# Optimization experiments

Measured on AMD Instinct MI355X. Metric: run time of the kernel, lower is better.

The kernel has to match this reference:

```python
import jax, jax.numpy as jnp
import numpy as np

B, S, D = 4, 2048, 512
H, DK = 8, 64
LN_EPS = 1e-5


def setup_inputs() -> dict:
    key = jax.random.key(0)
    ks = jax.random.split(key, 10)
    scale = 1.0 / np.sqrt(D)
    inp = {
        "input_Q": jax.random.normal(ks[0], (B, S, D), jnp.float32),
        "input_K": jax.random.normal(ks[1], (B, S, D), jnp.float32),
        "input_V": jax.random.normal(ks[2], (B, S, D), jnp.float32),
        # causal mask: True = masked (upper triangle), broadcast to batch
        "attn_mask": jnp.broadcast_to(
            jnp.triu(jnp.ones((S, S), jnp.bool_), k=1), (B, S, S)
        ),
        # Linear(d_model, d_k*n_heads, bias=False) weights, stored as [in, out]
        "W_Q": jax.random.normal(ks[3], (D, H * DK), jnp.float32) * scale,
        "W_K": jax.random.normal(ks[4], (D, H * DK), jnp.float32) * scale,
        "W_V": jax.random.normal(ks[5], (D, H * DK), jnp.float32) * scale,
        "W_fc": jax.random.normal(ks[6], (H * DK, D), jnp.float32) * scale,
        "ln_gamma": jnp.ones((D,), jnp.float32),
        "ln_beta": jnp.zeros((D,), jnp.float32),
    }
    return inp


def reference(input_Q, input_K, input_V, attn_mask, W_Q, W_K, W_V, W_fc, ln_gamma, ln_beta):
    # projections -> [B, H, S, DK]
    q = (input_Q @ W_Q).reshape(B, S, H, DK).transpose(0, 2, 1, 3)
    k = (input_K @ W_K).reshape(B, S, H, DK).transpose(0, 2, 1, 3)
    v = (input_V @ W_V).reshape(B, S, H, DK).transpose(0, 2, 1, 3)

    # scores: [B, H, S, S]
    scores = jnp.einsum("bhqd,bhkd->bhqk", q, k) / jnp.sqrt(jnp.float32(DK))
    scores = jnp.where(attn_mask[:, None, :, :], jnp.float32(-1e9), scores)
    attn = jax.nn.softmax(scores, axis=-1)

    # context: [B, S, H*DK]
    context = jnp.einsum("bhqk,bhkd->bhqd", attn, v)
    context = context.transpose(0, 2, 1, 3).reshape(B, S, H * DK)

    output = context @ W_fc + input_Q  # residual

    # LayerNorm over last dim
    mu = jnp.mean(output, axis=-1, keepdims=True)
    var = jnp.var(output, axis=-1, keepdims=True)
    return (output - mu) / jnp.sqrt(var + LN_EPS) * ln_gamma + ln_beta
```

## Files before the change

kernel.cpp:

```cpp
#include <hip/hip_runtime.h>
#include <hip/hip_bf16.h>
#include <stdint.h>

#define DEV __device__ __forceinline__

using f32x4  = __attribute__((ext_vector_type(4))) float;
using bf16x8 = __attribute__((ext_vector_type(8))) short;
using u16x4  = __attribute__((ext_vector_type(4))) unsigned short;
using u32x4  = __attribute__((ext_vector_type(4))) uint32_t;

DEV uint16_t f2b(float f) {
  uint32_t u = __builtin_bit_cast(uint32_t, f);
  uint32_t r = u + 0x7FFFu + ((u >> 16) & 1u);
  return (uint16_t)(r >> 16);
}

DEV uint32_t cvtpk(float lo, float hi) {
  uint32_t r;
  asm("v_cvt_pk_bf16_f32 %0, %1, %2" : "=v"(r) : "v"(lo), "v"(hi));
  return r;
}

DEV void gload16(const void* g, void* l) {
  __builtin_amdgcn_global_load_lds((__attribute__((address_space(1))) void*)g,
                                   (__attribute__((address_space(3))) void*)l,
                                   16, 0, 0);
}

DEV bf16x8 ldsfrag(const uint16_t* base, int row, int cb) {
  int b = row * 128 + (cb ^ ((row & 7) << 4));
  return *(const bf16x8*)((const uint8_t*)base + b);
}

DEV f32x4 MFMA(bf16x8 a, bf16x8 b, f32x4 c) {
  return __builtin_amdgcn_mfma_f32_16x16x32_bf16(a, b, c, 0, 0, 0);
}

__global__ void k_convert3(const float* __restrict__ A0, const float* __restrict__ A1,
                           const float* __restrict__ A2, uint16_t* __restrict__ O0,
                           uint16_t* __restrict__ O1, uint16_t* __restrict__ O2) {
  const int z = blockIdx.z;
  const float* in = (z == 0) ? A0 : (z == 1) ? A1 : A2;
  uint16_t* out = (z == 0) ? O0 : (z == 1) ? O1 : O2;
  int i = blockIdx.x * blockDim.x + threadIdx.x;
  int stride = gridDim.x * blockDim.x;
  for (; i < 1048576; i += stride) {
    f32x4 v = ((const f32x4*)in)[i];
    u16x4 o;
    o[0] = f2b(v[0]); o[1] = f2b(v[1]); o[2] = f2b(v[2]); o[3] = f2b(v[3]);
    ((u16x4*)out)[i] = o;
  }
}

__global__ void k_wtrans4(const float* __restrict__ W0, const float* __restrict__ W1,
                          const float* __restrict__ W2, const float* __restrict__ W3,
                          uint16_t* __restrict__ WtBase, float scale0) {
  __shared__ float t[32][33];
  const int z = blockIdx.z;
  const float* W = (z == 0) ? W0 : (z == 1) ? W1 : (z == 2) ? W2 : W3;
  const float scale = (z == 0) ? scale0 : 1.0f;
  uint16_t* Wt = WtBase + (size_t)z * 262144;
  int tx = threadIdx.x, ty = threadIdx.y;
  int n0 = blockIdx.x * 32, k0 = blockIdx.y * 32;
#pragma unroll
  for (int i = 0; i < 4; ++i)
    t[ty + 8 * i][tx] = W[(size_t)(k0 + ty + 8 * i) * 512 + n0 + tx];
  __syncthreads();
#pragma unroll
  for (int i = 0; i < 4; ++i)
    Wt[(size_t)(n0 + ty + 8 * i) * 512 + k0 + tx] = f2b(t[tx][ty + 8 * i] * scale);
}

DEV void stage_gemm(const uint8_t* Ab, const uint8_t* Bb, int m0, int n0, int kt,
                    uint16_t* As, uint16_t* Bs, int wid, int l8, int cb0) {
#pragma unroll
  for (int i = 0; i < 4; ++i) {
    int inst = wid + i * 4;
    int row = inst * 8 + l8;
    int cbs = cb0 ^ ((row & 7) << 4);
    gload16(Ab + (size_t)(m0 + row) * 1024 + kt * 128 + cbs, (uint8_t*)As + inst * 1024);
  }
#pragma unroll
  for (int i = 0; i < 2; ++i) {
    int inst = wid + i * 4;
    int row = inst * 8 + l8;
    int cbs = cb0 ^ ((row & 7) << 4);
    gload16(Bb + (size_t)(n0 + row) * 1024 + kt * 128 + cbs, (uint8_t*)Bs + inst * 1024);
  }
}

__global__ __launch_bounds__(256) void k_gemm_qkv(const uint16_t* __restrict__ A0,
                                                  const uint16_t* __restrict__ A1,
                                                  const uint16_t* __restrict__ A2,
                                                  const uint16_t* __restrict__ WtBase,
                                                  uint16_t* __restrict__ O0,
                                                  uint16_t* __restrict__ O1,
                                                  uint16_t* __restrict__ O2, int zbase) {
  __shared__ uint16_t As[2][8192];
  __shared__ uint16_t Bs[2][4096];
  const int z = blockIdx.z + zbase;
  const uint16_t* A = (z == 0) ? A0 : (z == 1) ? A1 : A2;
  uint16_t* out = (z == 0) ? O0 : (z == 1) ? O1 : O2;
  const uint8_t* Ab = (const uint8_t*)A;
  const uint8_t* Bb = (const uint8_t*)(WtBase + (size_t)z * 262144);
  const int tid = threadIdx.x, lane = tid & 63, wid = tid >> 6;
  const int g = lane >> 4, c16 = lane & 15;
  const int wm = wid & 1, wn = wid >> 1;
  const int m0 = blockIdx.x * 128, n0 = blockIdx.y * 64;
  const int l8 = lane >> 3, cb0 = (lane & 7) << 4;

  f32x4 acc[4][2] = {};

  stage_gemm(Ab, Bb, m0, n0, 0, As[0], Bs[0], wid, l8, cb0);
  __syncthreads();

  for (int kt = 0; kt < 8; ++kt) {
    const int cur = kt & 1;
    if (kt < 7)
      stage_gemm(Ab, Bb, m0, n0, kt + 1, As[cur ^ 1], Bs[cur ^ 1], wid, l8, cb0);
    const uint16_t* Ac = As[cur];
    const uint16_t* Bc = Bs[cur];
#pragma unroll
    for (int ks = 0; ks < 2; ++ks) {
      int cb = ks * 64 + (g << 4);
      bf16x8 af[4], bfr[2];
#pragma unroll
      for (int mi = 0; mi < 4; ++mi) af[mi] = ldsfrag(Ac, wm * 64 + mi * 16 + c16, cb);
#pragma unroll
      for (int ni = 0; ni < 2; ++ni) bfr[ni] = ldsfrag(Bc, wn * 32 + ni * 16 + c16, cb);
#pragma unroll
      for (int mi = 0; mi < 4; ++mi)
#pragma unroll
        for (int ni = 0; ni < 2; ++ni)
          acc[mi][ni] = MFMA(af[mi], bfr[ni], acc[mi][ni]);
    }
    __syncthreads();
  }

  const int lm = g * 4;
  if (z != 2) {
#pragma unroll
    for (int mi = 0; mi < 4; ++mi)
#pragma unroll
      for (int ni = 0; ni < 2; ++ni)
#pragma unroll
        for (int r = 0; r < 4; ++r) {
          int m = m0 + wm * 64 + mi * 16 + lm + r;
          int n = n0 + wn * 32 + ni * 16 + c16;
          size_t a = (size_t)((m >> 11) * 8 + (n >> 6)) * 131072 + (size_t)(m & 2047) * 64 + (n & 63);
          out[a] = f2b(acc[mi][ni][r]);
        }
  } else {
#pragma unroll
    for (int mi = 0; mi < 4; ++mi)
#pragma unroll
      for (int ni = 0; ni < 2; ++ni) {
        int m = m0 + wm * 64 + mi * 16 + lm;
        int n = n0 + wn * 32 + ni * 16 + c16;
        u16x4 w;
#pragma unroll
        for (int r = 0; r < 4; ++r) w[r] = f2b(acc[mi][ni][r]);
        size_t a = (size_t)((m >> 11) * 8 + (n >> 6)) * 131072 + (size_t)(n & 63) * 2048 + (m & 2047);
        *(u16x4*)(out + a) = w;
      }
  }
}

__global__ __launch_bounds__(256) void k_gemm_fc(const uint16_t* __restrict__ A,
                                                 const uint16_t* __restrict__ Bt,
                                                 float* __restrict__ out) {
  __shared__ uint16_t As[2][8192];
  __shared__ uint16_t Bs[2][4096];
  const int tid = threadIdx.x, lane = tid & 63, wid = tid >> 6;
  const int g = lane >> 4, c16 = lane & 15;
  const int wm = wid & 1, wn = wid >> 1;
  const int m0 = blockIdx.x * 128, n0 = blockIdx.y * 64;
  const uint8_t* Ab = (const uint8_t*)A;
  const uint8_t* Bb = (const uint8_t*)Bt;
  const int l8 = lane >> 3, cb0 = (lane & 7) << 4;

  f32x4 acc[4][2] = {};

  stage_gemm(Ab, Bb, m0, n0, 0, As[0], Bs[0], wid, l8, cb0);
  __syncthreads();

  for (int kt = 0; kt < 8; ++kt) {
    const int cur = kt & 1;
    if (kt < 7)
      stage_gemm(Ab, Bb, m0, n0, kt + 1, As[cur ^ 1], Bs[cur ^ 1], wid, l8, cb0);
    const uint16_t* Ac = As[cur];
    const uint16_t* Bc = Bs[cur];
#pragma unroll
    for (int ks = 0; ks < 2; ++ks) {
      int cb = ks * 64 + (g << 4);
      bf16x8 af[4], bfr[2];
#pragma unroll
      for (int mi = 0; mi < 4; ++mi) af[mi] = ldsfrag(Ac, wm * 64 + mi * 16 + c16, cb);
#pragma unroll
      for (int ni = 0; ni < 2; ++ni) bfr[ni] = ldsfrag(Bc, wn * 32 + ni * 16 + c16, cb);
#pragma unroll
      for (int mi = 0; mi < 4; ++mi)
#pragma unroll
        for (int ni = 0; ni < 2; ++ni)
          acc[mi][ni] = MFMA(af[mi], bfr[ni], acc[mi][ni]);
    }
    __syncthreads();
  }

  const int lm = g * 4;
#pragma unroll
  for (int mi = 0; mi < 4; ++mi)
#pragma unroll
    for (int ni = 0; ni < 2; ++ni)
#pragma unroll
      for (int r = 0; r < 4; ++r) {
        int m = m0 + wm * 64 + mi * 16 + lm + r;
        int n = n0 + wn * 32 + ni * 16 + c16;
        out[(size_t)m * 512 + n] = acc[mi][ni][r];
      }
}

DEV void stageK(const uint8_t* kb, int kt, uint16_t* Ks, int wid, int l8, int cb0) {
#pragma unroll
  for (int i = 0; i < 2; ++i) {
    int inst = wid + i * 4;
    int rho = inst * 8 + l8;
    int f = rho >> 4, g2 = (rho >> 2) & 3, r = rho & 3;
    int s_loc = ((f & 1) << 5) | (g2 << 3) | ((f >> 1) << 2) | r;
    int cbs = cb0 ^ ((rho & 7) << 4);
    gload16(kb + (size_t)(kt * 64 + s_loc) * 128 + cbs, (uint8_t*)Ks + inst * 1024);
  }
}
DEV void stageV(const uint8_t* vb, int kt, uint16_t* Vs, int wid, int l8, int cb0) {
#pragma unroll
  for (int i = 0; i < 2; ++i) {
    int inst = wid + i * 4;
    int row = inst * 8 + l8;
    int cbs = cb0 ^ ((row & 7) << 4);
    gload16(vb + (size_t)row * 4096 + (size_t)kt * 128 + cbs, (uint8_t*)Vs + inst * 1024);
  }
}

__global__ __launch_bounds__(256) void k_attn(const uint16_t* __restrict__ qg,
                                              const uint16_t* __restrict__ kg,
                                              const uint16_t* __restrict__ vtg,
                                              uint16_t* __restrict__ ctxg) {
  const int x = blockIdx.x, bh = blockIdx.y;
  const int gx = (x & 1) ? (x >> 1) : 31 - (x >> 1);
  const int qi = ((bh >> 3) & 1) ? 31 - gx : gx;

  const int tid = threadIdx.x, lane = tid & 63, wid = tid >> 6;
  const int g = lane >> 4, qcol = lane & 15;
  __shared__ uint16_t smem[4 * 4096];
  const uint8_t* qb = (const uint8_t*)(qg + (size_t)bh * 131072);
  const uint8_t* kb = (const uint8_t*)(kg + (size_t)bh * 131072);
  const uint8_t* vb = (const uint8_t*)(vtg + (size_t)bh * 131072);
  const int l8 = lane >> 3, cb0 = (lane & 7) << 4;
  const int qrow_w = qi * 64 + wid * 16;

  bf16x8 qf[2];
  {
    const uint8_t* qrow = qb + (size_t)(qrow_w + qcol) * 128;
    qf[0] = *(const bf16x8*)(qrow + (g << 4));
    qf[1] = *(const bf16x8*)(qrow + 64 + (g << 4));
  }

  stageK(kb, 0, smem, wid, l8, cb0);
  stageV(vb, 0, smem + 8192, wid, l8, cb0);
  __syncthreads();

  bf16x8 ones;
#pragma unroll
  for (int j = 0; j < 8; ++j) ones[j] = (short)0x3F80;

  f32x4 oacc[4] = {};
  f32x4 lacc = {};
  const int nkt = qi + 1;

  for (int kt = 0; kt < nkt; ++kt) {
    const int cur = kt & 1;
    if (kt + 1 < nkt) {
      stageK(kb, kt + 1, smem + ((cur ^ 1) << 12), wid, l8, cb0);
      stageV(vb, kt + 1, smem + 8192 + ((cur ^ 1) << 12), wid, l8, cb0);
    }
    const uint16_t* Kc = smem + (cur << 12);
    const uint16_t* Vc = smem + 8192 + (cur << 12);

    f32x4 sacc[4] = {};
#pragma unroll
    for (int ks2 = 0; ks2 < 2; ++ks2) {
      int cb = ks2 * 64 + (g << 4);
#pragma unroll
      for (int sf = 0; sf < 4; ++sf) {
        bf16x8 kf = ldsfrag(Kc, sf * 16 + qcol, cb);
        sacc[sf] = MFMA(kf, qf[ks2], sacc[sf]);
      }
    }

    if (kt * 64 + 63 > qrow_w) {
      int q_glob = qrow_w + qcol;
#pragma unroll
      for (int sf = 0; sf < 4; ++sf)
#pragma unroll
        for (int r = 0; r < 4; ++r) {
          int s_glob = kt * 64 + (((sf & 1) << 5) | (g << 3) | ((sf >> 1) << 2) | r);
          if (s_glob > q_glob) sacc[sf][r] = -1e30f;
        }
    }

    float p[4][4];
#pragma unroll
    for (int sf = 0; sf < 4; ++sf)
#pragma unroll
      for (int r = 0; r < 4; ++r) p[sf][r] = __builtin_amdgcn_exp2f(sacc[sf][r]);

#pragma unroll
    for (int ks = 0; ks < 2; ++ks) {
      u32x4 tv;
      tv[0] = cvtpk(p[ks][0], p[ks][1]);
      tv[1] = cvtpk(p[ks][2], p[ks][3]);
      tv[2] = cvtpk(p[2 + ks][0], p[2 + ks][1]);
      tv[3] = cvtpk(p[2 + ks][2], p[2 + ks][3]);
      bf16x8 pb = __builtin_bit_cast(bf16x8, tv);
      lacc = MFMA(ones, pb, lacc);
#pragma unroll
      for (int dkf = 0; dkf < 4; ++dkf) {
        bf16x8 vf = ldsfrag(Vc, dkf * 16 + qcol, ks * 64 + (g << 4));
        oacc[dkf] = MFMA(vf, pb, oacc[dkf]);
      }
    }
    __syncthreads();
  }

  uint16_t* Os = smem + wid * 1024;
  {
    float iv = 1.f / lacc[0];
    int q_l = qcol;
#pragma unroll
    for (int dkf = 0; dkf < 4; ++dkf) {
      u16x4 w;
#pragma unroll
      for (int r = 0; r < 4; ++r) w[r] = f2b(oacc[dkf][r] * iv);
      int dkb = dkf * 32 + g * 8;
      int bo = q_l * 128 + (dkb ^ ((q_l & 7) << 4));
      *(u16x4*)((uint8_t*)Os + bo) = w;
    }
  }
  __syncthreads();
  const int bb = bh >> 3, hh = bh & 7;
#pragma unroll
  for (int j = 0; j < 2; ++j) {
    int lin = j * 1024 + lane * 16;
    int q_l = lin >> 7;
    int cb = lin & 127;
    int bo = q_l * 128 + (cb ^ ((q_l & 7) << 4));
    bf16x8 val = *(const bf16x8*)((const uint8_t*)(smem + wid * 1024) + bo);
    size_t ga = (size_t)(bb * 2048 + qrow_w + q_l) * 512 + hh * 64 + (cb >> 1);
    *(bf16x8*)(ctxg + ga) = val;
  }
}

__global__ __launch_bounds__(256) void k_ln(const float* __restrict__ fc,
                                            const float* __restrict__ resid,
                                            const float* __restrict__ gamma,
                                            const float* __restrict__ beta,
                                            float* __restrict__ out) {
  int row = blockIdx.x * 4 + (threadIdx.x >> 6);
  int lane = threadIdx.x & 63;
  const float* fr = fc + (size_t)row * 512 + lane * 8;
  const float* rr = resid + (size_t)row * 512 + lane * 8;
  f32x4 a = *(const f32x4*)fr;
  f32x4 b = *(const f32x4*)(fr + 4);
  f32x4 c = *(const f32x4*)rr;
  f32x4 d = *(const f32x4*)(rr + 4);
  float y[8];
#pragma unroll
  for (int j = 0; j < 4; ++j) { y[j] = a[j] + c[j]; y[4 + j] = b[j] + d[j]; }
  float s = 0.f, s2 = 0.f;
#pragma unroll
  for (int j = 0; j < 8; ++j) { s += y[j]; s2 = fmaf(y[j], y[j], s2); }
#pragma unroll
  for (int off = 1; off < 64; off <<= 1) {
    s += __shfl_xor(s, off);
    s2 += __shfl_xor(s2, off);
  }
  float mean = s * (1.f / 512.f);
  float var = s2 * (1.f / 512.f) - mean * mean;
  float rstd = rsqrtf(var + 1e-5f);
  f32x4 o0, o1;
#pragma unroll
  for (int j = 0; j < 4; ++j) {
    o0[j] = (y[j] - mean) * rstd * gamma[lane * 8 + j] + beta[lane * 8 + j];
    o1[j] = (y[4 + j] - mean) * rstd * gamma[lane * 8 + 4 + j] + beta[lane * 8 + 4 + j];
  }
  float* op = out + (size_t)row * 512 + lane * 8;
  *(f32x4*)op = o0;
  *(f32x4*)(op + 4) = o1;
}

extern "C" void kernel_launch(void* const* d_in, const int* in_sizes, int n_in,
                              void* d_out, int out_size, void* d_ws, size_t ws_size,
                              hipStream_t stream) {
  const float* inQ = (const float*)d_in[0];
  const float* inK = (const float*)d_in[1];
  const float* inV = (const float*)d_in[2];
  const float* Wq = (const float*)d_in[4];
  const float* Wk = (const float*)d_in[5];
  const float* Wv = (const float*)d_in[6];
  const float* Wfc = (const float*)d_in[7];
  const float* gamma = (const float*)d_in[8];
  const float* beta = (const float*)d_in[9];
  uint8_t* ws = (uint8_t*)d_ws;
  const size_t MB = 1048576;

  uint16_t* Wt  = (uint16_t*)(ws + 0);
  uint16_t* Xb0 = (uint16_t*)(ws + 2 * MB);
  uint16_t* Xb1 = (uint16_t*)(ws + 10 * MB);
  uint16_t* Xb2 = (uint16_t*)(ws + 18 * MB);
  const bool fused = ws_size >= 52 * MB;

  uint16_t *Qb, *Kb, *Vtb, *Ctx;
  float* Fc;
  if (fused) {
    Qb  = (uint16_t*)(ws + 26 * MB);
    Kb  = (uint16_t*)(ws + 34 * MB);
    Vtb = (uint16_t*)(ws + 42 * MB);
    Ctx = (uint16_t*)(ws + 2 * MB);
    Fc  = (float*)(ws + 10 * MB);
  } else {
    Qb  = (uint16_t*)(ws + 26 * MB);
    Kb  = (uint16_t*)(ws + 34 * MB);
    Vtb = (uint16_t*)(ws + 2 * MB);
    Ctx = (uint16_t*)(ws + 10 * MB);
    Fc  = (float*)(ws + 18 * MB);
  }
  float* out = (float*)d_out;

  dim3 b256(256);
  dim3 tb(32, 8), tg4(16, 16, 4);
  k_wtrans4<<<tg4, tb, 0, stream>>>(Wq, Wk, Wv, Wfc, Wt, 0.18033688011112042f);

  dim3 cg(1024, 1, 3);
  k_convert3<<<cg, b256, 0, stream>>>(inQ, inK, inV, Xb0, Xb1, Xb2);

  if (fused) {
    dim3 gq(64, 8, 3);
    k_gemm_qkv<<<gq, b256, 0, stream>>>(Xb0, Xb1, Xb2, Wt, Qb, Kb, Vtb, 0);
  } else {
    dim3 gq(64, 8, 1);
    k_gemm_qkv<<<gq, b256, 0, stream>>>(Xb0, Xb1, Xb2, Wt, Qb, Kb, Vtb, 0);
    k_gemm_qkv<<<gq, b256, 0, stream>>>(Xb0, Xb1, Xb2, Wt, Qb, Kb, Vtb, 1);
    k_gemm_qkv<<<gq, b256, 0, stream>>>(Xb0, Xb1, Xb2, Wt, Qb, Kb, Vtb, 2);
  }

  dim3 ag(32, 32);
  k_attn<<<ag, b256, 0, stream>>>(Qb, Kb, Vtb, Ctx);

  dim3 gg(64, 8);
  k_gemm_fc<<<gg, b256, 0, stream>>>(Ctx, Wt + 3 * 262144, Fc);
  k_ln<<<2048, b256, 0, stream>>>(Fc, inQ, gamma, beta, out);
}
```

Measured before the change: 92.46 us.

## Double attention query tile to 128 rows so each wave handles two chunks

The attention kernel now gives each block 128 query rows instead of 64, with each wave processing two 16-row query chunks. Every K and V fragment read from LDS feeds two MFMAs, and the number of K/V tile loads per output row is halved. The grid drops to 16x32 blocks and the causal tile order is simplified to a reversal on alternate batch pairs. In exchange, accumulator registers double, there are fewer blocks to balance the triangular workload, and more fully masked work is computed near the diagonal.

```diff
diff --git a/kernel.cpp b/kernel.cpp
--- a/kernel.cpp
+++ b/kernel.cpp
@@ -246,8 +246,7 @@
                                               const uint16_t* __restrict__ vtg,
                                               uint16_t* __restrict__ ctxg) {
   const int x = blockIdx.x, bh = blockIdx.y;
-  const int gx = (x & 1) ? (x >> 1) : 31 - (x >> 1);
-  const int qi = ((bh >> 3) & 1) ? 31 - gx : gx;
+  const int qi = (bh & 16) ? 15 - x : x;
 
   const int tid = threadIdx.x, lane = tid & 63, wid = tid >> 6;
   const int g = lane >> 4, qcol = lane & 15;
@@ -256,13 +255,14 @@
   const uint8_t* kb = (const uint8_t*)(kg + (size_t)bh * 131072);
   const uint8_t* vb = (const uint8_t*)(vtg + (size_t)bh * 131072);
   const int l8 = lane >> 3, cb0 = (lane & 7) << 4;
-  const int qrow_w = qi * 64 + wid * 16;
-
-  bf16x8 qf[2];
-  {
-    const uint8_t* qrow = qb + (size_t)(qrow_w + qcol) * 128;
-    qf[0] = *(const bf16x8*)(qrow + (g << 4));
-    qf[1] = *(const bf16x8*)(qrow + 64 + (g << 4));
+  const int qrow_w = qi * 128 + wid * 32;
+
+  bf16x8 qf[2][2];
+#pragma unroll
+  for (int qc = 0; qc < 2; ++qc) {
+    const uint8_t* qrow = qb + (size_t)(qrow_w + qc * 16 + qcol) * 128;
+    qf[qc][0] = *(const bf16x8*)(qrow + (g << 4));
+    qf[qc][1] = *(const bf16x8*)(qrow + 64 + (g << 4));
   }
 
   stageK(kb, 0, smem, wid, l8, cb0);
@@ -273,9 +273,9 @@
 #pragma unroll
   for (int j = 0; j < 8; ++j) ones[j] = (short)0x3F80;
 
-  f32x4 oacc[4] = {};
-  f32x4 lacc = {};
-  const int nkt = qi + 1;
+  f32x4 oacc[4][2] = {};
+  f32x4 lacc[2] = {};
+  const int nkt = 2 * qi + 2;
 
   for (int kt = 0; kt < nkt; ++kt) {
     const int cur = kt & 1;
@@ -286,61 +286,75 @@
     const uint16_t* Kc = smem + (cur << 12);
     const uint16_t* Vc = smem + 8192 + (cur << 12);
 
-    f32x4 sacc[4] = {};
+    f32x4 sacc[4][2] = {};
 #pragma unroll
     for (int ks2 = 0; ks2 < 2; ++ks2) {
       int cb = ks2 * 64 + (g << 4);
 #pragma unroll
       for (int sf = 0; sf < 4; ++sf) {
         bf16x8 kf = ldsfrag(Kc, sf * 16 + qcol, cb);
-        sacc[sf] = MFMA(kf, qf[ks2], sacc[sf]);
+        sacc[sf][0] = MFMA(kf, qf[0][ks2], sacc[sf][0]);
+        sacc[sf][1] = MFMA(kf, qf[1][ks2], sacc[sf][1]);
       }
     }
 
     if (kt * 64 + 63 > qrow_w) {
-      int q_glob = qrow_w + qcol;
+#pragma unroll
+      for (int qc = 0; qc < 2; ++qc) {
+        int q_glob = qrow_w + qc * 16 + qcol;
+#pragma unroll
+        for (int sf = 0; sf < 4; ++sf)
+#pragma unroll
+          for (int r = 0; r < 4; ++r) {
+            int s_glob = kt * 64 + (((sf & 1) << 5) | (g << 3) | ((sf >> 1) << 2) | r);
+            if (s_glob > q_glob) sacc[sf][qc][r] = -1e30f;
+          }
+      }
+    }
+
+    float p[2][4][4];
+#pragma unroll
+    for (int qc = 0; qc < 2; ++qc)
 #pragma unroll
       for (int sf = 0; sf < 4; ++sf)
 #pragma unroll
-        for (int r = 0; r < 4; ++r) {
-          int s_glob = kt * 64 + (((sf & 1) << 5) | (g << 3) | ((sf >> 1) << 2) | r);
-          if (s_glob > q_glob) sacc[sf][r] = -1e30f;
-        }
-    }
-
-    float p[4][4];
-#pragma unroll
-    for (int sf = 0; sf < 4; ++sf)
-#pragma unroll
-      for (int r = 0; r < 4; ++r) p[sf][r] = __builtin_amdgcn_exp2f(sacc[sf][r]);
+        for (int r = 0; r < 4; ++r) p[qc][sf][r] = __builtin_amdgcn_exp2f(sacc[sf][qc][r]);
 
 #pragma unroll
     for (int ks = 0; ks < 2; ++ks) {
-      u32x4 tv;
-      tv[0] = cvtpk(p[ks][0], p[ks][1]);
-      tv[1] = cvtpk(p[ks][2], p[ks][3]);
-      tv[2] = cvtpk(p[2 + ks][0], p[2 + ks][1]);
-      tv[3] = cvtpk(p[2 + ks][2], p[2 + ks][3]);
-      bf16x8 pb = __builtin_bit_cast(bf16x8, tv);
-      lacc = MFMA(ones, pb, lacc);
+      u32x4 tv0, tv1;
+      tv0[0] = cvtpk(p[0][ks][0], p[0][ks][1]);
+      tv0[1] = cvtpk(p[0][ks][2], p[0][ks][3]);
+      tv0[2] = cvtpk(p[0][2 + ks][0], p[0][2 + ks][1]);
+      tv0[3] = cvtpk(p[0][2 + ks][2], p[0][2 + ks][3]);
+      tv1[0] = cvtpk(p[1][ks][0], p[1][ks][1]);
+      tv1[1] = cvtpk(p[1][ks][2], p[1][ks][3]);
+      tv1[2] = cvtpk(p[1][2 + ks][0], p[1][2 + ks][1]);
+      tv1[3] = cvtpk(p[1][2 + ks][2], p[1][2 + ks][3]);
+      bf16x8 pb0 = __builtin_bit_cast(bf16x8, tv0);
+      bf16x8 pb1 = __builtin_bit_cast(bf16x8, tv1);
+      lacc[0] = MFMA(ones, pb0, lacc[0]);
+      lacc[1] = MFMA(ones, pb1, lacc[1]);
 #pragma unroll
       for (int dkf = 0; dkf < 4; ++dkf) {
         bf16x8 vf = ldsfrag(Vc, dkf * 16 + qcol, ks * 64 + (g << 4));
-        oacc[dkf] = MFMA(vf, pb, oacc[dkf]);
+        oacc[dkf][0] = MFMA(vf, pb0, oacc[dkf][0]);
+        oacc[dkf][1] = MFMA(vf, pb1, oacc[dkf][1]);
       }
     }
     __syncthreads();
   }
 
-  uint16_t* Os = smem + wid * 1024;
-  {
-    float iv = 1.f / lacc[0];
-    int q_l = qcol;
+  uint16_t* Os = smem + wid * 2048;
+#pragma unroll
+  for (int qc = 0; qc < 2; ++qc) {
+    float iv = 1.f / lacc[qc][0];
+    int q_l = qc * 16 + qcol;
 #pragma unroll
     for (int dkf = 0; dkf < 4; ++dkf) {
       u16x4 w;
 #pragma unroll
-      for (int r = 0; r < 4; ++r) w[r] = f2b(oacc[dkf][r] * iv);
+      for (int r = 0; r < 4; ++r) w[r] = f2b(oacc[dkf][qc][r] * iv);
       int dkb = dkf * 32 + g * 8;
       int bo = q_l * 128 + (dkb ^ ((q_l & 7) << 4));
       *(u16x4*)((uint8_t*)Os + bo) = w;
@@ -349,12 +363,12 @@
   __syncthreads();
   const int bb = bh >> 3, hh = bh & 7;
 #pragma unroll
-  for (int j = 0; j < 2; ++j) {
+  for (int j = 0; j < 4; ++j) {
     int lin = j * 1024 + lane * 16;
     int q_l = lin >> 7;
     int cb = lin & 127;
     int bo = q_l * 128 + (cb ^ ((q_l & 7) << 4));
-    bf16x8 val = *(const bf16x8*)((const uint8_t*)(smem + wid * 1024) + bo);
+    bf16x8 val = *(const bf16x8*)((const uint8_t*)(smem + wid * 2048) + bo);
     size_t ga = (size_t)(bb * 2048 + qrow_w + q_l) * 512 + hh * 64 + (cb >> 1);
     *(bf16x8*)(ctxg + ga) = val;
   }
@@ -453,7 +467,7 @@
     k_gemm_qkv<<<gq, b256, 0, stream>>>(Xb0, Xb1, Xb2, Wt, Qb, Kb, Vtb, 2);
   }
 
-  dim3 ag(32, 32);
+  dim3 ag(16, 32);
   k_attn<<<ag, b256, 0, stream>>>(Qb, Kb, Vtb, Ctx);
 
   dim3 gg(64, 8);
```

Result: slower. 97.49 us (+5.4%).

## Pair causal attention query tiles per block and store FC output as bf16

Applied to the files above, without the earlier changes.

Each attention block now processes two query tiles, x and 31-x, in sequence, so every block does the same total causal work, and the grid is halved to 16x32. This is meant to remove load imbalance and tail effects from uneven causal tile lengths. Separately, the FC GEMM writes its result as bf16 instead of fp32 and LayerNorm reads bf16, which halves that intermediate traffic at some cost in precision before the residual add. Halving the grid to 512 blocks may leave compute units underused, and each block runs longer.

```diff
diff --git a/kernel.cpp b/kernel.cpp
--- a/kernel.cpp
+++ b/kernel.cpp
@@ -7,12 +7,16 @@
 using f32x4  = __attribute__((ext_vector_type(4))) float;
 using bf16x8 = __attribute__((ext_vector_type(8))) short;
 using u16x4  = __attribute__((ext_vector_type(4))) unsigned short;
+using u16x8  = __attribute__((ext_vector_type(8))) unsigned short;
 using u32x4  = __attribute__((ext_vector_type(4))) uint32_t;
 
 DEV uint16_t f2b(float f) {
   uint32_t u = __builtin_bit_cast(uint32_t, f);
   uint32_t r = u + 0x7FFFu + ((u >> 16) & 1u);
   return (uint16_t)(r >> 16);
+}
+DEV float b2f(uint16_t h) {
+  return __builtin_bit_cast(float, (uint32_t)h << 16);
 }
 
 DEV uint32_t cvtpk(float lo, float hi) {
@@ -168,7 +172,7 @@
 
 __global__ __launch_bounds__(256) void k_gemm_fc(const uint16_t* __restrict__ A,
                                                  const uint16_t* __restrict__ Bt,
-                                                 float* __restrict__ out) {
+                                                 uint16_t* __restrict__ out) {
   __shared__ uint16_t As[2][8192];
   __shared__ uint16_t Bs[2][4096];
   const int tid = threadIdx.x, lane = tid & 63, wid = tid >> 6;
@@ -216,7 +220,7 @@
       for (int r = 0; r < 4; ++r) {
         int m = m0 + wm * 64 + mi * 16 + lm + r;
         int n = n0 + wn * 32 + ni * 16 + c16;
-        out[(size_t)m * 512 + n] = acc[mi][ni][r];
+        out[(size_t)m * 512 + n] = f2b(acc[mi][ni][r]);
       }
 }
 
@@ -246,9 +250,6 @@
                                               const uint16_t* __restrict__ vtg,
                                               uint16_t* __restrict__ ctxg) {
   const int x = blockIdx.x, bh = blockIdx.y;
-  const int gx = (x & 1) ? (x >> 1) : 31 - (x >> 1);
-  const int qi = ((bh >> 3) & 1) ? 31 - gx : gx;
-
   const int tid = threadIdx.x, lane = tid & 63, wid = tid >> 6;
   const int g = lane >> 4, qcol = lane & 15;
   __shared__ uint16_t smem[4 * 4096];
@@ -256,126 +257,130 @@
   const uint8_t* kb = (const uint8_t*)(kg + (size_t)bh * 131072);
   const uint8_t* vb = (const uint8_t*)(vtg + (size_t)bh * 131072);
   const int l8 = lane >> 3, cb0 = (lane & 7) << 4;
-  const int qrow_w = qi * 64 + wid * 16;
-
-  bf16x8 qf[2];
-  {
-    const uint8_t* qrow = qb + (size_t)(qrow_w + qcol) * 128;
-    qf[0] = *(const bf16x8*)(qrow + (g << 4));
-    qf[1] = *(const bf16x8*)(qrow + 64 + (g << 4));
-  }
-
-  stageK(kb, 0, smem, wid, l8, cb0);
-  stageV(vb, 0, smem + 8192, wid, l8, cb0);
-  __syncthreads();
+  const int bb = bh >> 3, hh = bh & 7;
 
   bf16x8 ones;
 #pragma unroll
   for (int j = 0; j < 8; ++j) ones[j] = (short)0x3F80;
 
-  f32x4 oacc[4] = {};
-  f32x4 lacc = {};
-  const int nkt = qi + 1;
-
-  for (int kt = 0; kt < nkt; ++kt) {
-    const int cur = kt & 1;
-    if (kt + 1 < nkt) {
-      stageK(kb, kt + 1, smem + ((cur ^ 1) << 12), wid, l8, cb0);
-      stageV(vb, kt + 1, smem + 8192 + ((cur ^ 1) << 12), wid, l8, cb0);
-    }
-    const uint16_t* Kc = smem + (cur << 12);
-    const uint16_t* Vc = smem + 8192 + (cur << 12);
-
-    f32x4 sacc[4] = {};
-#pragma unroll
-    for (int ks2 = 0; ks2 < 2; ++ks2) {
-      int cb = ks2 * 64 + (g << 4);
-#pragma unroll
-      for (int sf = 0; sf < 4; ++sf) {
-        bf16x8 kf = ldsfrag(Kc, sf * 16 + qcol, cb);
-        sacc[sf] = MFMA(kf, qf[ks2], sacc[sf]);
-      }
-    }
-
-    if (kt * 64 + 63 > qrow_w) {
-      int q_glob = qrow_w + qcol;
+  for (int phase = 0; phase < 2; ++phase) {
+    const int qi = phase ? 31 - x : x;
+    const int qrow_w = qi * 64 + wid * 16;
+
+    bf16x8 qf[2];
+    {
+      const uint8_t* qrow = qb + (size_t)(qrow_w + qcol) * 128;
+      qf[0] = *(const bf16x8*)(qrow + (g << 4));
+      qf[1] = *(const bf16x8*)(qrow + 64 + (g << 4));
+    }
+
+    stageK(kb, 0, smem, wid, l8, cb0);
+    stageV(vb, 0, smem + 8192, wid, l8, cb0);
+    __syncthreads();
+
+    f32x4 oacc[4] = {};
+    f32x4 lacc = {};
+    const int nkt = qi + 1;
+
+    for (int kt = 0; kt < nkt; ++kt) {
+      const int cur = kt & 1;
+      if (kt + 1 < nkt) {
+        stageK(kb, kt + 1, smem + ((cur ^ 1) << 12), wid, l8, cb0);
+        stageV(vb, kt + 1, smem + 8192 + ((cur ^ 1) << 12), wid, l8, cb0);
+      }
+      const uint16_t* Kc = smem + (cur << 12);
+      const uint16_t* Vc = smem + 8192 + (cur << 12);
+
+      f32x4 sacc[4] = {};
+#pragma unroll
+      for (int ks2 = 0; ks2 < 2; ++ks2) {
+        int cb = ks2 * 64 + (g << 4);
+#pragma unroll
+        for (int sf = 0; sf < 4; ++sf) {
+          bf16x8 kf = ldsfrag(Kc, sf * 16 + qcol, cb);
+          sacc[sf] = MFMA(kf, qf[ks2], sacc[sf]);
+        }
+      }
+
+      if (kt * 64 + 63 > qrow_w) {
+        int q_glob = qrow_w + qcol;
+#pragma unroll
+        for (int sf = 0; sf < 4; ++sf)
+#pragma unroll
+          for (int r = 0; r < 4; ++r) {
+            int s_glob = kt * 64 + (((sf & 1) << 5) | (g << 3) | ((sf >> 1) << 2) | r);
+            if (s_glob > q_glob) sacc[sf][r] = -1e30f;
+          }
+      }
+
+      float p[4][4];
 #pragma unroll
       for (int sf = 0; sf < 4; ++sf)
 #pragma unroll
-        for (int r = 0; r < 4; ++r) {
-          int s_glob = kt * 64 + (((sf & 1) << 5) | (g << 3) | ((sf >> 1) << 2) | r);
-          if (s_glob > q_glob) sacc[sf][r] = -1e30f;
+        for (int r = 0; r < 4; ++r) p[sf][r] = __builtin_amdgcn_exp2f(sacc[sf][r]);
+
+#pragma unroll
+      for (int ks = 0; ks < 2; ++ks) {
+        u32x4 tv;
+        tv[0] = cvtpk(p[ks][0], p[ks][1]);
+        tv[1] = cvtpk(p[ks][2], p[ks][3]);
+        tv[2] = cvtpk(p[2 + ks][0], p[2 + ks][1]);
+        tv[3] = cvtpk(p[2 + ks][2], p[2 + ks][3]);
+        bf16x8 pb = __builtin_bit_cast(bf16x8, tv);
+        lacc = MFMA(ones, pb, lacc);
+#pragma unroll
+        for (int dkf = 0; dkf < 4; ++dkf) {
+          bf16x8 vf = ldsfrag(Vc, dkf * 16 + qcol, ks * 64 + (g << 4));
+          oacc[dkf] = MFMA(vf, pb, oacc[dkf]);
         }
-    }
-
-    float p[4][4];
-#pragma unroll
-    for (int sf = 0; sf < 4; ++sf)
-#pragma unroll
-      for (int r = 0; r < 4; ++r) p[sf][r] = __builtin_amdgcn_exp2f(sacc[sf][r]);
-
-#pragma unroll
-    for (int ks = 0; ks < 2; ++ks) {
-      u32x4 tv;
-      tv[0] = cvtpk(p[ks][0], p[ks][1]);
-      tv[1] = cvtpk(p[ks][2], p[ks][3]);
-      tv[2] = cvtpk(p[2 + ks][0], p[2 + ks][1]);
-      tv[3] = cvtpk(p[2 + ks][2], p[2 + ks][3]);
-      bf16x8 pb = __builtin_bit_cast(bf16x8, tv);
-      lacc = MFMA(ones, pb, lacc);
+      }
+      __syncthreads();
+    }
+
+    uint16_t* Os = smem + wid * 1024;
+    {
+      float iv = 1.f / lacc[0];
+      int q_l = qcol;
 #pragma unroll
       for (int dkf = 0; dkf < 4; ++dkf) {
-        bf16x8 vf = ldsfrag(Vc, dkf * 16 + qcol, ks * 64 + (g << 4));
-        oacc[dkf] = MFMA(vf, pb, oacc[dkf]);
+        u16x4 w;
+#pragma unroll
+        for (int r = 0; r < 4; ++r) w[r] = f2b(oacc[dkf][r] * iv);
+        int dkb = dkf * 32 + g * 8;
+        int bo = q_l * 128 + (dkb ^ ((q_l & 7) << 4));
+        *(u16x4*)((uint8_t*)Os + bo) = w;
       }
     }
     __syncthreads();
-  }
-
-  uint16_t* Os = smem + wid * 1024;
-  {
-    float iv = 1.f / lacc[0];
-    int q_l = qcol;
-#pragma unroll
-    for (int dkf = 0; dkf < 4; ++dkf) {
-      u16x4 w;
-#pragma unroll
-      for (int r = 0; r < 4; ++r) w[r] = f2b(oacc[dkf][r] * iv);
-      int dkb = dkf * 32 + g * 8;
-      int bo = q_l * 128 + (dkb ^ ((q_l & 7) << 4));
-      *(u16x4*)((uint8_t*)Os + bo) = w;
-    }
-  }
-  __syncthreads();
-  const int bb = bh >> 3, hh = bh & 7;
-#pragma unroll
-  for (int j = 0; j < 2; ++j) {
-    int lin = j * 1024 + lane * 16;
-    int q_l = lin >> 7;
-    int cb = lin & 127;
-    int bo = q_l * 128 + (cb ^ ((q_l & 7) << 4));
-    bf16x8 val = *(const bf16x8*)((const uint8_t*)(smem + wid * 1024) + bo);
-    size_t ga = (size_t)(bb * 2048 + qrow_w + q_l) * 512 + hh * 64 + (cb >> 1);
-    *(bf16x8*)(ctxg + ga) = val;
-  }
-}
-
-__global__ __launch_bounds__(256) void k_ln(const float* __restrict__ fc,
+#pragma unroll
+    for (int j = 0; j < 2; ++j) {
+      int lin = j * 1024 + lane * 16;
+      int q_l = lin >> 7;
+      int cb = lin & 127;
+      int bo = q_l * 128 + (cb ^ ((q_l & 7) << 4));
+      bf16x8 val = *(const bf16x8*)((const uint8_t*)(smem + wid * 1024) + bo);
+      size_t ga = (size_t)(bb * 2048 + qrow_w + q_l) * 512 + hh * 64 + (cb >> 1);
+      *(bf16x8*)(ctxg + ga) = val;
+    }
+    __syncthreads();
+  }
+}
+
+__global__ __launch_bounds__(256) void k_ln(const uint16_t* __restrict__ fc,
                                             const float* __restrict__ resid,
                                             const float* __restrict__ gamma,
                                             const float* __restrict__ beta,
                                             float* __restrict__ out) {
   int row = blockIdx.x * 4 + (threadIdx.x >> 6);
   int lane = threadIdx.x & 63;
-  const float* fr = fc + (size_t)row * 512 + lane * 8;
+  const uint16_t* fr = fc + (size_t)row * 512 + lane * 8;
   const float* rr = resid + (size_t)row * 512 + lane * 8;
-  f32x4 a = *(const f32x4*)fr;
-  f32x4 b = *(const f32x4*)(fr + 4);
+  u16x8 fv = *(const u16x8*)fr;
   f32x4 c = *(const f32x4*)rr;
   f32x4 d = *(const f32x4*)(rr + 4);
   float y[8];
 #pragma unroll
-  for (int j = 0; j < 4; ++j) { y[j] = a[j] + c[j]; y[4 + j] = b[j] + d[j]; }
+  for (int j = 0; j < 4; ++j) { y[j] = b2f(fv[j]) + c[j]; y[4 + j] = b2f(fv[4 + j]) + d[j]; }
   float s = 0.f, s2 = 0.f;
 #pragma unroll
   for (int j = 0; j < 8; ++j) { s += y[j]; s2 = fmaf(y[j], y[j], s2); }
@@ -419,20 +424,19 @@
   uint16_t* Xb2 = (uint16_t*)(ws + 18 * MB);
   const bool fused = ws_size >= 52 * MB;
 
-  uint16_t *Qb, *Kb, *Vtb, *Ctx;
-  float* Fc;
+  uint16_t *Qb, *Kb, *Vtb, *Ctx, *Fc;
   if (fused) {
     Qb  = (uint16_t*)(ws + 26 * MB);
     Kb  = (uint16_t*)(ws + 34 * MB);
     Vtb = (uint16_t*)(ws + 42 * MB);
     Ctx = (uint16_t*)(ws + 2 * MB);
-    Fc  = (float*)(ws + 10 * MB);
+    Fc  = (uint16_t*)(ws + 10 * MB);
   } else {
     Qb  = (uint16_t*)(ws + 26 * MB);
     Kb  = (uint16_t*)(ws + 34 * MB);
     Vtb = (uint16_t*)(ws + 2 * MB);
     Ctx = (uint16_t*)(ws + 10 * MB);
-    Fc  = (float*)(ws + 18 * MB);
+    Fc  = (uint16_t*)(ws + 18 * MB);
   }
   float* out = (float*)d_out;
 
@@ -453,7 +457,7 @@
     k_gemm_qkv<<<gq, b256, 0, stream>>>(Xb0, Xb1, Xb2, Wt, Qb, Kb, Vtb, 2);
   }
 
-  dim3 ag(32, 32);
+  dim3 ag(16, 32);
   k_attn<<<ag, b256, 0, stream>>>(Qb, Kb, Vtb, Ctx);
 
   dim3 gg(64, 8);
```

Measured after the change: 100.5 us. +8.6%, slower.
